# Optimization experiments

Hardware: AMD Instinct MI355X
Metric: run time of the kernel (lower is better)

Reference implementation:

```python
import jax, jax.numpy as jnp
import numpy as np

SIGMA = 7.0
KERNEL_SIZE = int(2 * np.ceil(SIGMA * 2) + 1)  # 29
PAD = (KERNEL_SIZE - 1) // 2  # 14


def _gaussian_kernel2d():
    variance = SIGMA ** 2
    coords = jnp.arange(KERNEL_SIZE, dtype=jnp.float32)
    mean = (KERNEL_SIZE - 1) / 2.0
    xg, yg = jnp.meshgrid(coords, coords, indexing='xy')
    k = jnp.exp(-((xg - mean) ** 2 + (yg - mean) ** 2) / (2.0 * variance))
    k = k / (2.0 * np.pi * variance)
    return k / k.sum()  # [K, K]


def setup_inputs() -> dict:
    key = jax.random.key(0)
    x = jax.random.normal(key, (8, 64, 256, 256), dtype=jnp.float32)
    return {"x": x}


def reference(x):
    channels = x.shape[1]
    k2d = _gaussian_kernel2d().astype(x.dtype)
    # depthwise weights: [C, 1, K, K] (OIHW with feature_group_count=C)
    w = jnp.broadcast_to(k2d, (channels, 1, KERNEL_SIZE, KERNEL_SIZE))
    xp = jnp.pad(x, ((0, 0), (0, 0), (PAD, PAD), (PAD, PAD)), mode='reflect')
    out = jax.lax.conv_general_dilated(
        xp, w,
        window_strides=(1, 1),
        padding='VALID',
        dimension_numbers=('NCHW', 'OIHW', 'NCHW'),
        feature_group_count=channels,
    )
    return out
```

## Files before the change

kernel.cpp:

```cpp
#include <hip/hip_runtime.h>

#define IMG   256
#define ROWS  32
#define KS    29
#define PAD   14
#define LDSS  284

static constexpr float GK[15] = {
    1.0f,        0.98984780f, 0.96000544f, 0.91225408f, 0.84936581f,
    0.77483743f, 0.69256933f, 0.60653066f, 0.52045012f, 0.43756474f,
    0.36044779f, 0.29092381f, 0.23006630f, 0.17826398f, 0.13533528f
};
static constexpr float GSUM =
    GK[0] + 2.0f * (GK[1] + GK[2] + GK[3] + GK[4] + GK[5] + GK[6] + GK[7] +
                    GK[8] + GK[9] + GK[10] + GK[11] + GK[12] + GK[13] + GK[14]);
static constexpr float WT[29] = {
    GK[14]/GSUM, GK[13]/GSUM, GK[12]/GSUM, GK[11]/GSUM, GK[10]/GSUM, GK[9]/GSUM, GK[8]/GSUM,
    GK[7]/GSUM,  GK[6]/GSUM,  GK[5]/GSUM,  GK[4]/GSUM,  GK[3]/GSUM,  GK[2]/GSUM, GK[1]/GSUM,
    GK[0]/GSUM,
    GK[1]/GSUM,  GK[2]/GSUM,  GK[3]/GSUM,  GK[4]/GSUM,  GK[5]/GSUM,  GK[6]/GSUM, GK[7]/GSUM,
    GK[8]/GSUM,  GK[9]/GSUM,  GK[10]/GSUM, GK[11]/GSUM, GK[12]/GSUM, GK[13]/GSUM, GK[14]/GSUM
};

__device__ __forceinline__ int refl(int p) {
    int a = p < 0 ? -p : p;
    int b = 2 * (IMG - 1) - a;
    return a < b ? a : b;
}

__global__ __launch_bounds__(512, 8)
void gauss_v4(const float* __restrict__ x, float* __restrict__ out) {
    __shared__ float s[ROWS * LDSS];

    const int t   = threadIdx.x;
    const int img = blockIdx.y;
    const int y0  = blockIdx.x * ROWS;

    const float* __restrict__ src = x   + (size_t)img * (IMG * IMG);
    float*       __restrict__ dst = out + (size_t)img * (IMG * IMG);

    {
        const int cq   = t & 63;
        const int rg   = t >> 6;
        const int c0   = cq * 4;
        const int brow = y0 + rg * 4 - PAD;

        float4 acc[4];
        #pragma unroll
        for (int j = 0; j < 4; ++j) acc[j] = make_float4(0.f, 0.f, 0.f, 0.f);

        if (brow >= 0 && brow + 31 < IMG) {
            const float* p = src + (size_t)brow * IMG + c0;
            #pragma unroll
            for (int sdx = 0; sdx < 32; ++sdx) {
                const float4 v = *(const float4*)(p + sdx * IMG);
                #pragma unroll
                for (int j = 0; j < 4; ++j) {
                    const int k = sdx - j;
                    if (k >= 0 && k < KS) {
                        acc[j].x += WT[k] * v.x;
                        acc[j].y += WT[k] * v.y;
                        acc[j].z += WT[k] * v.z;
                        acc[j].w += WT[k] * v.w;
                    }
                }
            }
        } else {
            #pragma unroll
            for (int sdx = 0; sdx < 32; ++sdx) {
                const float4 v = *(const float4*)(src + (size_t)refl(brow + sdx) * IMG + c0);
                #pragma unroll
                for (int j = 0; j < 4; ++j) {
                    const int k = sdx - j;
                    if (k >= 0 && k < KS) {
                        acc[j].x += WT[k] * v.x;
                        acc[j].y += WT[k] * v.y;
                        acc[j].z += WT[k] * v.z;
                        acc[j].w += WT[k] * v.w;
                    }
                }
            }
        }

        #pragma unroll
        for (int j = 0; j < 4; ++j) {
            float* row = &s[(rg * 4 + j) * LDSS + PAD + c0];
            *(float2*)(row)     = make_float2(acc[j].x, acc[j].y);
            *(float2*)(row + 2) = make_float2(acc[j].z, acc[j].w);
        }
        if (c0 <= PAD || c0 >= IMG - 1 - PAD - 3) {
            #pragma unroll
            for (int q = 0; q < 4; ++q) {
                const int c = c0 + q;
                if (c >= 1 && c <= PAD) {
                    #pragma unroll
                    for (int j = 0; j < 4; ++j) {
                        const float v = q == 0 ? acc[j].x : q == 1 ? acc[j].y : q == 2 ? acc[j].z : acc[j].w;
                        s[(rg * 4 + j) * LDSS + (PAD - c)] = v;
                    }
                } else if (c >= IMG - 1 - PAD && c <= IMG - 2) {
                    #pragma unroll
                    for (int j = 0; j < 4; ++j) {
                        const float v = q == 0 ? acc[j].x : q == 1 ? acc[j].y : q == 2 ? acc[j].z : acc[j].w;
                        s[(rg * 4 + j) * LDSS + (2 * (IMG - 1) + PAD - c)] = v;
                    }
                }
            }
        }
    }
    __syncthreads();

    {
        const int row = t & 31;
        const int cg  = t >> 5;
        const int c0  = cg * 16;

        float acc[16];
        #pragma unroll
        for (int c = 0; c < 16; ++c) acc[c] = 0.f;

        const float4* srow = (const float4*)&s[row * LDSS + c0];
        #pragma unroll
        for (int m = 0; m < 11; ++m) {
            const float4 v4 = srow[m];
            #pragma unroll
            for (int q = 0; q < 4; ++q) {
                const int p = 4 * m + q;
                const float v = q == 0 ? v4.x : q == 1 ? v4.y : q == 2 ? v4.z : v4.w;
                #pragma unroll
                for (int c = 0; c < 16; ++c) {
                    const int k = p - c;
                    if (k >= 0 && k < KS) acc[c] += WT[k] * v;
                }
            }
        }

        float4* orow = (float4*)&dst[(size_t)(y0 + row) * IMG + c0];
        #pragma unroll
        for (int m = 0; m < 4; ++m)
            orow[m] = make_float4(acc[4*m+0], acc[4*m+1], acc[4*m+2], acc[4*m+3]);
    }
}

extern "C" void kernel_launch(void* const* d_in, const int* in_sizes, int n_in,
                              void* d_out, int out_size, void* d_ws, size_t ws_size,
                              hipStream_t stream) {
    const float* x = (const float*)d_in[0];
    float* out = (float*)d_out;
    const int images = in_sizes[0] / (IMG * IMG);
    dim3 grid(IMG / ROWS, images);
    gauss_v4<<<grid, dim3(512), 0, stream>>>(x, out);
}
```

Measured before the change: 84.00 us.

## Halve block size, compute 8 rows per thread, restructure horizontal pass

Cuts the block from 512 to 256 threads, each thread now computing 8 output rows in the vertical pass instead of 4. This lowers redundant global reads per output row (36 loads for 8 rows versus 32 for 4), and loads are batched in chunks of 12 float4s to raise memory-level parallelism. The horizontal pass now gives each thread 4 adjacent columns across 8 rows, reading 9 float4s from LDS per row, with a wider padded LDS row aligned for float4 stores. Register pressure rises and the horizontal pass reuses fewer loaded values, so it issues more LDS reads per output.

```diff
diff --git a/kernel.cpp b/kernel.cpp
--- a/kernel.cpp
+++ b/kernel.cpp
@@ -1,10 +1,11 @@
 #include <hip/hip_runtime.h>
 
 #define IMG   256
-#define ROWS  32
+#define SROWS 32
 #define KS    29
 #define PAD   14
-#define LDSS  284
+#define LDSS  292
+#define MOFF  16
 
 static constexpr float GK[15] = {
     1.0f,        0.98984780f, 0.96000544f, 0.91225408f, 0.84936581f,
@@ -28,81 +29,95 @@
     return a < b ? a : b;
 }
 
-__global__ __launch_bounds__(512, 8)
-void gauss_v4(const float* __restrict__ x, float* __restrict__ out) {
-    __shared__ float s[ROWS * LDSS];
+__global__ __launch_bounds__(256, 4)
+void gauss_v6(const float* __restrict__ x, float* __restrict__ out) {
+    __shared__ float s[SROWS * LDSS];
 
     const int t   = threadIdx.x;
     const int img = blockIdx.y;
-    const int y0  = blockIdx.x * ROWS;
+    const int y0  = blockIdx.x * SROWS;
 
     const float* __restrict__ src = x   + (size_t)img * (IMG * IMG);
     float*       __restrict__ dst = out + (size_t)img * (IMG * IMG);
 
+    const int cq = t & 63;
+    const int rg = t >> 6;
+    const int c0 = cq * 4;
+
     {
-        const int cq   = t & 63;
-        const int rg   = t >> 6;
-        const int c0   = cq * 4;
-        const int brow = y0 + rg * 4 - PAD;
+        const int brow = y0 + rg * 8 - PAD;
 
-        float4 acc[4];
+        float4 acc[8];
         #pragma unroll
-        for (int j = 0; j < 4; ++j) acc[j] = make_float4(0.f, 0.f, 0.f, 0.f);
+        for (int j = 0; j < 8; ++j) acc[j] = make_float4(0.f, 0.f, 0.f, 0.f);
 
-        if (brow >= 0 && brow + 31 < IMG) {
+        const bool interior = (brow >= 0) && (brow + 35 < IMG);
+        if (interior) {
             const float* p = src + (size_t)brow * IMG + c0;
             #pragma unroll
-            for (int sdx = 0; sdx < 32; ++sdx) {
-                const float4 v = *(const float4*)(p + sdx * IMG);
+            for (int ch = 0; ch < 3; ++ch) {
+                float4 v[12];
                 #pragma unroll
-                for (int j = 0; j < 4; ++j) {
-                    const int k = sdx - j;
-                    if (k >= 0 && k < KS) {
-                        acc[j].x += WT[k] * v.x;
-                        acc[j].y += WT[k] * v.y;
-                        acc[j].z += WT[k] * v.z;
-                        acc[j].w += WT[k] * v.w;
+                for (int i = 0; i < 12; ++i)
+                    v[i] = *(const float4*)(p + (ch * 12 + i) * IMG);
+                #pragma unroll
+                for (int i = 0; i < 12; ++i) {
+                    const int sdx = ch * 12 + i;
+                    #pragma unroll
+                    for (int j = 0; j < 8; ++j) {
+                        const int k = sdx - j;
+                        if (k >= 0 && k < KS) {
+                            acc[j].x += WT[k] * v[i].x;
+                            acc[j].y += WT[k] * v[i].y;
+                            acc[j].z += WT[k] * v[i].z;
+                            acc[j].w += WT[k] * v[i].w;
+                        }
                     }
                 }
             }
         } else {
             #pragma unroll
-            for (int sdx = 0; sdx < 32; ++sdx) {
-                const float4 v = *(const float4*)(src + (size_t)refl(brow + sdx) * IMG + c0);
+            for (int ch = 0; ch < 3; ++ch) {
+                float4 v[12];
                 #pragma unroll
-                for (int j = 0; j < 4; ++j) {
-                    const int k = sdx - j;
-                    if (k >= 0 && k < KS) {
-                        acc[j].x += WT[k] * v.x;
-                        acc[j].y += WT[k] * v.y;
-                        acc[j].z += WT[k] * v.z;
-                        acc[j].w += WT[k] * v.w;
+                for (int i = 0; i < 12; ++i)
+                    v[i] = *(const float4*)(src + (size_t)refl(brow + ch * 12 + i) * IMG + c0);
+                #pragma unroll
+                for (int i = 0; i < 12; ++i) {
+                    const int sdx = ch * 12 + i;
+                    #pragma unroll
+                    for (int j = 0; j < 8; ++j) {
+                        const int k = sdx - j;
+                        if (k >= 0 && k < KS) {
+                            acc[j].x += WT[k] * v[i].x;
+                            acc[j].y += WT[k] * v[i].y;
+                            acc[j].z += WT[k] * v[i].z;
+                            acc[j].w += WT[k] * v[i].w;
+                        }
                     }
                 }
             }
         }
 
         #pragma unroll
-        for (int j = 0; j < 4; ++j) {
-            float* row = &s[(rg * 4 + j) * LDSS + PAD + c0];
-            *(float2*)(row)     = make_float2(acc[j].x, acc[j].y);
-            *(float2*)(row + 2) = make_float2(acc[j].z, acc[j].w);
-        }
-        if (c0 <= PAD || c0 >= IMG - 1 - PAD - 3) {
+        for (int j = 0; j < 8; ++j)
+            *(float4*)&s[(rg * 8 + j) * LDSS + MOFF + c0] = acc[j];
+
+        if (c0 <= PAD || c0 + 3 >= IMG - 1 - PAD) {
             #pragma unroll
             for (int q = 0; q < 4; ++q) {
                 const int c = c0 + q;
                 if (c >= 1 && c <= PAD) {
                     #pragma unroll
-                    for (int j = 0; j < 4; ++j) {
+                    for (int j = 0; j < 8; ++j) {
                         const float v = q == 0 ? acc[j].x : q == 1 ? acc[j].y : q == 2 ? acc[j].z : acc[j].w;
-                        s[(rg * 4 + j) * LDSS + (PAD - c)] = v;
+                        s[(rg * 8 + j) * LDSS + (MOFF - c)] = v;
                     }
                 } else if (c >= IMG - 1 - PAD && c <= IMG - 2) {
                     #pragma unroll
-                    for (int j = 0; j < 4; ++j) {
+                    for (int j = 0; j < 8; ++j) {
                         const float v = q == 0 ? acc[j].x : q == 1 ? acc[j].y : q == 2 ? acc[j].z : acc[j].w;
-                        s[(rg * 4 + j) * LDSS + (2 * (IMG - 1) + PAD - c)] = v;
+                        s[(rg * 8 + j) * LDSS + (MOFF + 2 * (IMG - 1) - c)] = v;
                     }
                 }
             }
@@ -111,34 +126,35 @@
     __syncthreads();
 
     {
-        const int row = t & 31;
-        const int cg  = t >> 5;
-        const int c0  = cg * 16;
+        #pragma unroll
+        for (int r = 0; r < 8; ++r) {
+            const int row = rg * 8 + r;
+            const float4* w = (const float4*)&s[row * LDSS + c0];
+            float4 v[9];
+            #pragma unroll
+            for (int m = 0; m < 9; ++m) v[m] = w[m];
 
-        float acc[16];
-        #pragma unroll
-        for (int c = 0; c < 16; ++c) acc[c] = 0.f;
-
-        const float4* srow = (const float4*)&s[row * LDSS + c0];
-        #pragma unroll
-        for (int m = 0; m < 11; ++m) {
-            const float4 v4 = srow[m];
+            float4 o = make_float4(0.f, 0.f, 0.f, 0.f);
             #pragma unroll
-            for (int q = 0; q < 4; ++q) {
-                const int p = 4 * m + q;
-                const float v = q == 0 ? v4.x : q == 1 ? v4.y : q == 2 ? v4.z : v4.w;
+            for (int m = 0; m < 9; ++m) {
                 #pragma unroll
-                for (int c = 0; c < 16; ++c) {
-                    const int k = p - c;
-                    if (k >= 0 && k < KS) acc[c] += WT[k] * v;
+                for (int q = 0; q < 4; ++q) {
+                    const int p = 4 * m + q;
+                    const float val = q == 0 ? v[m].x : q == 1 ? v[m].y : q == 2 ? v[m].z : v[m].w;
+                    #pragma unroll
+                    for (int c = 0; c < 4; ++c) {
+                        const int k = p - c - 2;
+                        if (k >= 0 && k < KS) {
+                            if (c == 0) o.x += WT[k] * val;
+                            else if (c == 1) o.y += WT[k] * val;
+                            else if (c == 2) o.z += WT[k] * val;
+                            else o.w += WT[k] * val;
+                        }
+                    }
                 }
             }
+            *(float4*)&dst[(size_t)(y0 + row) * IMG + c0] = o;
         }
-
-        float4* orow = (float4*)&dst[(size_t)(y0 + row) * IMG + c0];
-        #pragma unroll
-        for (int m = 0; m < 4; ++m)
-            orow[m] = make_float4(acc[4*m+0], acc[4*m+1], acc[4*m+2], acc[4*m+3]);
     }
 }
 
@@ -148,6 +164,6 @@
     const float* x = (const float*)d_in[0];
     float* out = (float*)d_out;
     const int images = in_sizes[0] / (IMG * IMG);
-    dim3 grid(IMG / ROWS, images);
-    gauss_v4<<<grid, dim3(512), 0, stream>>>(x, out);
+    dim3 grid(IMG / SROWS, images);
+    gauss_v6<<<grid, dim3(256), 0, stream>>>(x, out);
 }
```

Measured after the change: 96.76 us. 1.15x slower.
